# Kernel optimization log

Hardware: AMD Instinct MI355X
Metric: run time of the kernel (lower is better)

## Reference

```python
import jax, jax.numpy as jnp
import numpy as np


def setup_inputs() -> dict:
    key = jax.random.key(0)
    ks = jax.random.split(key, 5)
    B, H, W, C, R = 4, 64, 64, 256, 32
    x = jax.random.normal(ks[0], (B, H, W, C), dtype=jnp.float32)
    # 1x1 conv kernels stored as [C_in, C_out] matrices (equivalent math)
    w_f = jax.random.normal(ks[1], (C, R), dtype=jnp.float32) * (1.0 / np.sqrt(C))
    w_g = jax.random.normal(ks[2], (C, R), dtype=jnp.float32) * (1.0 / np.sqrt(C))
    w_h = jax.random.normal(ks[3], (C, R), dtype=jnp.float32) * (1.0 / np.sqrt(C))
    w_v = jax.random.normal(ks[4], (R, C), dtype=jnp.float32) * (1.0 / np.sqrt(R))
    gamma = jnp.zeros((1,), dtype=jnp.float32)
    return {"x": x, "w_f": w_f, "w_g": w_g, "w_h": w_h, "w_v": w_v, "gamma": gamma}


def reference(x, w_f, w_g, w_h, w_v, gamma):
    B, H, W, C = x.shape
    N = H * W
    xt = x.reshape(B, N, C)                       # flatten spatial tokens
    f = jnp.einsum('bnc,cr->bnr', xt, w_f)        # 1x1 conv == token-wise matmul
    g = jnp.einsum('bnc,cr->bnr', xt, w_g)
    h = jnp.einsum('bnc,cr->bnr', xt, w_h)
    scores = jnp.einsum('bnr,bmr->bnm', f, g)     # [B, N, N]
    # NOTE: original softmaxes over axis=1 (the query/row axis), not axis=-1
    attn = jax.nn.softmax(scores, axis=1)
    y = jnp.einsum('bnm,bmr->bnr', attn, h)       # [B, N, R]
    y = jnp.einsum('bnr,rc->bnc', y, w_v)         # output 1x1 conv
    y = y.reshape(B, H, W, C)
    return gamma * y + x
```

## Files before the change

kernel.cpp:

```cpp
#include <hip/hip_runtime.h>


#define BB 4
#define NN 4096
#define CC 256
#define RR 32
#define CSEG 4
#define MP 40
#define LOG2E 1.44269504088896340736f

typedef short short8 __attribute__((ext_vector_type(8)));
typedef unsigned short ushort8 __attribute__((ext_vector_type(8)));
typedef float floatx4 __attribute__((ext_vector_type(4)));

#define MFMA16 __builtin_amdgcn_mfma_f32_16x16x32_bf16

static __device__ __forceinline__ unsigned short f2bf(float f) {
  union { float f; unsigned u; } v; v.f = f;
  const unsigned r = v.u + 0x7fffu + ((v.u >> 16) & 1u);
  return (unsigned short)(r >> 16);
}
static __device__ __forceinline__ unsigned bfpack(float lo, float hi) {
  return __builtin_amdgcn_perm(__float_as_uint(hi), __float_as_uint(lo), 0x07060302u);
}

__global__ __launch_bounds__(256) void k_prep(
    const float* __restrict__ wf, const float* __restrict__ wg,
    const float* __restrict__ wh, const float* __restrict__ wv,
    unsigned short* __restrict__ wfrag, unsigned short* __restrict__ wvfrag) {
  const int idx = blockIdx.x * 256 + threadIdx.x;
  const int lane = (idx >> 3) & 63;
  const int j = idx & 7;
  const int col = lane & 15, q = lane >> 4;
  if (idx < 24576) {
    const int mat = idx >> 13;
    const int fid = (idx >> 9) & 15;
    const int kc = fid >> 1, nt = fid & 1;
    const float* w = (mat == 0) ? wf : ((mat == 1) ? wg : wh);
    wfrag[idx] = f2bf(w[(kc * 32 + q * 8 + j) * RR + nt * 16 + col]);
  } else {
    const int r = idx - 24576;
    const int t = (r >> 9) & 15;
    wvfrag[r] = f2bf(wv[(q * 8 + j) * CC + t * 16 + col]);
  }
}

__global__ __launch_bounds__(256) void k_fgh(
    const float* __restrict__ x, const unsigned short* __restrict__ wfrag,
    unsigned short* __restrict__ f16, unsigned short* __restrict__ g16,
    unsigned short* __restrict__ hT16) {
  __shared__ unsigned short wflds[24576];
  const int tid = threadIdx.x, lane = tid & 63, wave = tid >> 6;
  const int col = lane & 15, q = lane >> 4;
  {
    const uint4* src = (const uint4*)wfrag;
    uint4* dst = (uint4*)wflds;
#pragma unroll
    for (int i = 0; i < 12; ++i) dst[tid + i * 256] = src[tid + i * 256];
  }
  __syncthreads();
  const int t0 = blockIdx.x * 64 + wave * 16;
  short8 af[8];
  const float* xr = x + (long)(t0 + col) * CC + q * 8;
#pragma unroll
  for (int kc = 0; kc < 8; ++kc) {
    float tmp[8];
    *(float4*)(tmp) = *(const float4*)(xr + kc * 32);
    *(float4*)(tmp + 4) = *(const float4*)(xr + kc * 32 + 4);
    short8 o;
#pragma unroll
    for (int j = 0; j < 8; ++j) o[j] = (short)f2bf(tmp[j]);
    af[kc] = o;
  }
  const floatx4 zero = {0.f, 0.f, 0.f, 0.f};
  floatx4 acc[3][2];
#pragma unroll
  for (int m = 0; m < 3; ++m) { acc[m][0] = zero; acc[m][1] = zero; }
#pragma unroll
  for (int kc = 0; kc < 8; ++kc) {
#pragma unroll
    for (int mat = 0; mat < 3; ++mat) {
#pragma unroll
      for (int nt = 0; nt < 2; ++nt) {
        const short8 bf = *(const short8*)(wflds + (mat * 16 + kc * 2 + nt) * 512 + lane * 8);
        acc[mat][nt] = MFMA16(af[kc], bf, acc[mat][nt], 0, 0, 0);
      }
    }
  }
  const int b = t0 >> 12;
#pragma unroll
  for (int nt = 0; nt < 2; ++nt) {
#pragma unroll
    for (int r = 0; r < 4; ++r) {
      const int tok = t0 + q * 4 + r;
      const int n = nt * 16 + col;
      f16[(long)tok * RR + n] = f2bf(acc[0][nt][r] * LOG2E);
      g16[(long)tok * RR + n] = f2bf(acc[1][nt][r]);
      hT16[((long)b * RR + n) * NN + (tok & (NN - 1))] = f2bf(acc[2][nt][r]);
    }
  }
}

__global__ __launch_bounds__(256) void k_colsum(
    const unsigned short* __restrict__ f16, const unsigned short* __restrict__ g16,
    float* __restrict__ psum) {
  const int tid = threadIdx.x, lane = tid & 63, wave = tid >> 6;
  const int col = lane & 15, q = lane >> 4;
  const int mblk = blockIdx.x & 31;
  const int b = (blockIdx.x >> 5) & 3;
  const int seg = blockIdx.x >> 7;
  const int m0 = mblk * 128 + wave * 32;
  const short8 bg1 = *(const short8*)(g16 + ((long)(b * NN + m0 + col)) * RR + q * 8);
  const short8 bg2 = *(const short8*)(g16 + ((long)(b * NN + m0 + 16 + col)) * RR + q * 8);
  const floatx4 zero = {0.f, 0.f, 0.f, 0.f};
  float s1 = 0.f, s2 = 0.f;
  const unsigned short* fb = f16 + ((long)b * NN + seg * (NN / CSEG)) * RR;
#pragma unroll 4
  for (int n = 0; n < NN / CSEG; n += 16) {
    const short8 af = *(const short8*)(fb + (long)(n + col) * RR + q * 8);
    const floatx4 d1 = MFMA16(af, bg1, zero, 0, 0, 0);
    const floatx4 d2 = MFMA16(af, bg2, zero, 0, 0, 0);
    s1 += __builtin_amdgcn_exp2f(d1[0]) + __builtin_amdgcn_exp2f(d1[1]) +
          __builtin_amdgcn_exp2f(d1[2]) + __builtin_amdgcn_exp2f(d1[3]);
    s2 += __builtin_amdgcn_exp2f(d2[0]) + __builtin_amdgcn_exp2f(d2[1]) +
          __builtin_amdgcn_exp2f(d2[2]) + __builtin_amdgcn_exp2f(d2[3]);
  }
  s1 += __shfl_xor(s1, 16); s1 += __shfl_xor(s1, 32);
  s2 += __shfl_xor(s2, 16); s2 += __shfl_xor(s2, 32);
  if (lane < 16) {
    psum[(long)seg * (BB * NN) + b * NN + m0 + lane] = s1;
    psum[(long)seg * (BB * NN) + b * NN + m0 + 16 + lane] = s2;
  }
}

__global__ __launch_bounds__(256) void k_scaleh(
    const float* __restrict__ psum, unsigned short* __restrict__ hT16) {
  const long i8 = ((long)blockIdx.x * 256 + threadIdx.x) * 8;
  const int b = (int)(i8 >> 17);
  const int m = (int)(i8 & (NN - 1));
  float cs[8] = {0.f, 0.f, 0.f, 0.f, 0.f, 0.f, 0.f, 0.f};
#pragma unroll
  for (int sg = 0; sg < CSEG; ++sg) {
    const float* p = psum + (long)sg * (BB * NN) + b * NN + m;
    const float4 a = *(const float4*)p;
    const float4 c = *(const float4*)(p + 4);
    cs[0] += a.x; cs[1] += a.y; cs[2] += a.z; cs[3] += a.w;
    cs[4] += c.x; cs[5] += c.y; cs[6] += c.z; cs[7] += c.w;
  }
  const ushort8 hv = *(const ushort8*)(hT16 + i8);
  ushort8 o;
#pragma unroll
  for (int j = 0; j < 8; ++j) {
    const float h = __uint_as_float(((unsigned)hv[j]) << 16);
    o[j] = f2bf(h * __builtin_amdgcn_rcpf(cs[j]));
  }
  *(ushort8*)(hT16 + i8) = o;
}

#define C_ADDR(TN, TM) (((TN) + col) * MP + (TM) + q * 4)
__global__ __launch_bounds__(512, 4) void k_pvout(
    const unsigned short* __restrict__ f16, const unsigned short* __restrict__ g16,
    const unsigned short* __restrict__ hT16, const unsigned short* __restrict__ wvfrag,
    const float* __restrict__ x, const float* __restrict__ gamma,
    float* __restrict__ out) {
  __shared__ float ylds[8][32 * 36];
  __shared__ unsigned short pt_all[8][32 * MP];
  const int tid = threadIdx.x, lane = tid & 63, wave = tid >> 6;
  const int col = lane & 15, q = lane >> 4;
  const int b = blockIdx.x >> 7;
  const int t0 = (blockIdx.x & 127) * 32;
  const floatx4 zero = {0.f, 0.f, 0.f, 0.f};
  const short8 af1 = *(const short8*)(f16 + ((long)(b * NN + t0 + col)) * RR + q * 8);
  const short8 af2 = *(const short8*)(f16 + ((long)(b * NN + t0 + 16 + col)) * RR + q * 8);
  floatx4 a11 = zero, a12 = zero, a21 = zero, a22 = zero;
  unsigned short* pt = &pt_all[wave][0];
  const unsigned short* gb = g16 + (long)b * NN * RR;
  const unsigned short* hb = hT16 + (long)b * RR * NN;
  const int mq = wave * 512;
#pragma unroll 2
  for (int mi = 0; mi < 512; mi += 32) {
    const int m0 = mq + mi;
    const short8 bg1 = *(const short8*)(gb + (long)(m0 + col) * RR + q * 8);
    const short8 bg2 = *(const short8*)(gb + (long)(m0 + 16 + col) * RR + q * 8);
    const floatx4 d00 = MFMA16(bg1, af1, zero, 0, 0, 0);
    const floatx4 d01 = MFMA16(bg2, af1, zero, 0, 0, 0);
    const floatx4 d10 = MFMA16(bg1, af2, zero, 0, 0, 0);
    const floatx4 d11 = MFMA16(bg2, af2, zero, 0, 0, 0);
    float w0, w1, w2, w3;
    w0 = __builtin_amdgcn_exp2f(d00[0]); w1 = __builtin_amdgcn_exp2f(d00[1]);
    w2 = __builtin_amdgcn_exp2f(d00[2]); w3 = __builtin_amdgcn_exp2f(d00[3]);
    *(uint2*)(pt + C_ADDR(0, 0)) = make_uint2(bfpack(w0, w1), bfpack(w2, w3));
    w0 = __builtin_amdgcn_exp2f(d01[0]); w1 = __builtin_amdgcn_exp2f(d01[1]);
    w2 = __builtin_amdgcn_exp2f(d01[2]); w3 = __builtin_amdgcn_exp2f(d01[3]);
    *(uint2*)(pt + C_ADDR(0, 16)) = make_uint2(bfpack(w0, w1), bfpack(w2, w3));
    w0 = __builtin_amdgcn_exp2f(d10[0]); w1 = __builtin_amdgcn_exp2f(d10[1]);
    w2 = __builtin_amdgcn_exp2f(d10[2]); w3 = __builtin_amdgcn_exp2f(d10[3]);
    *(uint2*)(pt + C_ADDR(16, 0)) = make_uint2(bfpack(w0, w1), bfpack(w2, w3));
    w0 = __builtin_amdgcn_exp2f(d11[0]); w1 = __builtin_amdgcn_exp2f(d11[1]);
    w2 = __builtin_amdgcn_exp2f(d11[2]); w3 = __builtin_amdgcn_exp2f(d11[3]);
    *(uint2*)(pt + C_ADDR(16, 16)) = make_uint2(bfpack(w0, w1), bfpack(w2, w3));
    const short8 ap1 = *(const short8*)(pt + col * MP + q * 8);
    const short8 ap2 = *(const short8*)(pt + (col + 16) * MP + q * 8);
    const short8 bh1 = *(const short8*)(hb + (long)col * NN + m0 + q * 8);
    const short8 bh2 = *(const short8*)(hb + (long)(col + 16) * NN + m0 + q * 8);
    a11 = MFMA16(ap1, bh1, a11, 0, 0, 0);
    a12 = MFMA16(ap1, bh2, a12, 0, 0, 0);
    a21 = MFMA16(ap2, bh1, a21, 0, 0, 0);
    a22 = MFMA16(ap2, bh2, a22, 0, 0, 0);
  }
  {
    float* yp = &ylds[wave][0];
#pragma unroll
    for (int r = 0; r < 4; ++r) {
      yp[(q * 4 + r) * 36 + col] = a11[r];
      yp[(q * 4 + r) * 36 + col + 16] = a12[r];
      yp[(16 + q * 4 + r) * 36 + col] = a21[r];
      yp[(16 + q * 4 + r) * 36 + col + 16] = a22[r];
    }
  }
  __syncthreads();
  {
    const int tile = wave & 1, hh = wave >> 1;
    float s[8] = {0.f, 0.f, 0.f, 0.f, 0.f, 0.f, 0.f, 0.f};
#pragma unroll
    for (int w2 = 0; w2 < 8; ++w2) {
      const float* yp = &ylds[w2][(tile * 16 + col) * 36 + q * 8];
      const float4 u0 = *(const float4*)yp;
      const float4 u1 = *(const float4*)(yp + 4);
      s[0] += u0.x; s[1] += u0.y; s[2] += u0.z; s[3] += u0.w;
      s[4] += u1.x; s[5] += u1.y; s[6] += u1.z; s[7] += u1.w;
    }
    short8 ay;
#pragma unroll
    for (int j = 0; j < 8; ++j) ay[j] = (short)f2bf(s[j]);
    const float gm = gamma[0];
    float* sc = (float*)pt;
    const int row = lane >> 2, c4 = (lane & 3) * 4;
#pragma unroll
    for (int tp = 0; tp < 4; tp += 2) {
      const short8 bw0 = *(const short8*)(wvfrag + (hh * 4 + tp) * 512 + lane * 8);
      const short8 bw1 = *(const short8*)(wvfrag + (hh * 4 + tp + 1) * 512 + lane * 8);
      const floatx4 d0 = MFMA16(ay, bw0, zero, 0, 0, 0);
      const floatx4 d1 = MFMA16(ay, bw1, zero, 0, 0, 0);
#pragma unroll
      for (int r = 0; r < 4; ++r) {
        sc[(q * 4 + r) * 36 + col] = d0[r];
        sc[(q * 4 + r) * 36 + col + 16] = d1[r];
      }
#pragma unroll
      for (int j = 0; j < 2; ++j) {
        const float4 v = *(const float4*)(sc + row * 36 + c4 + j * 16);
        const long gidx = (long)(b * NN + t0 + tile * 16 + row) * CC +
                          hh * 64 + tp * 16 + j * 16 + c4;
        const float4 xv = *(const float4*)(x + gidx);
        float4 o;
        o.x = gm * v.x + xv.x; o.y = gm * v.y + xv.y;
        o.z = gm * v.z + xv.z; o.w = gm * v.w + xv.w;
        *(float4*)(out + gidx) = o;
      }
    }
  }
}

extern "C" void kernel_launch(void* const* d_in, const int* in_sizes, int n_in,
                              void* d_out, int out_size, void* d_ws, size_t ws_size,
                              hipStream_t stream) {
  const float* x = (const float*)d_in[0];
  const float* wf = (const float*)d_in[1];
  const float* wg = (const float*)d_in[2];
  const float* wh = (const float*)d_in[3];
  const float* wv = (const float*)d_in[4];
  const float* gamma = (const float*)d_in[5];
  float* out = (float*)d_out;

  unsigned short* f16 = (unsigned short*)d_ws;
  unsigned short* g16 = f16 + (long)BB * NN * RR;
  unsigned short* hT16 = g16 + (long)BB * NN * RR;
  unsigned short* wfrag = hT16 + (long)BB * NN * RR;
  unsigned short* wvfrag = wfrag + 24576;
  float* psum = (float*)(wvfrag + 8192);

  k_prep<<<128, 256, 0, stream>>>(wf, wg, wh, wv, wfrag, wvfrag);
  k_fgh<<<BB * NN / 64, 256, 0, stream>>>(x, wfrag, f16, g16, hT16);
  k_colsum<<<CSEG * BB * 32, 256, 0, stream>>>(f16, g16, psum);
  k_scaleh<<<BB * RR * NN / 2048, 256, 0, stream>>>(psum, hT16);
  k_pvout<<<BB * 128, 512, 0, stream>>>(f16, g16, hT16, wvfrag, x, gamma, out);
}
```

Before: 123.3 us.

## Feed exp scores directly from MFMA accumulators into PV MFMA, skipping LDS transpose

The P·V product now takes the exponentiated score accumulators straight from registers as A-operands of 16x16x16 bf16 MFMAs, so the per-iteration LDS store and reload of the P tile goes away. To match the register layout, the transposed h buffer is written in a permuted token order, and the column-sum normalisation kernel reads its sums with the same permutation. The cost is twice as many smaller-K MFMA instructions and a more intricate index mapping that must stay consistent across three kernels.

Result: no change. 125.0 us (+1.4%).

```diff
diff --git a/kernel.cpp b/kernel.cpp
--- a/kernel.cpp
+++ b/kernel.cpp
@@ -6,14 +6,15 @@
 #define CC 256
 #define RR 32
 #define CSEG 4
-#define MP 40
 #define LOG2E 1.44269504088896340736f
 
 typedef short short8 __attribute__((ext_vector_type(8)));
+typedef short short4v __attribute__((ext_vector_type(4)));
 typedef unsigned short ushort8 __attribute__((ext_vector_type(8)));
 typedef float floatx4 __attribute__((ext_vector_type(4)));
 
 #define MFMA16 __builtin_amdgcn_mfma_f32_16x16x32_bf16
+#define MFMA16K __builtin_amdgcn_mfma_f32_16x16x16bf16_1k
 
 static __device__ __forceinline__ unsigned short f2bf(float f) {
   union { float f; unsigned u; } v; v.f = f;
@@ -96,7 +97,9 @@
       const int n = nt * 16 + col;
       f16[(long)tok * RR + n] = f2bf(acc[0][nt][r] * LOG2E);
       g16[(long)tok * RR + n] = f2bf(acc[1][nt][r]);
-      hT16[((long)b * RR + n) * NN + (tok & (NN - 1))] = f2bf(acc[2][nt][r]);
+      const int tl = tok & (NN - 1);
+      const int sp = (tl & ~31) | (q << 3) | ((tl & 16) >> 2) | r;
+      hT16[((long)b * RR + n) * NN + sp] = f2bf(acc[2][nt][r]);
     }
   }
 }
@@ -138,12 +141,13 @@
   const long i8 = ((long)blockIdx.x * 256 + threadIdx.x) * 8;
   const int b = (int)(i8 >> 17);
   const int m = (int)(i8 & (NN - 1));
+  const int lo = (m & ~31) | ((m & 24) >> 1);
   float cs[8] = {0.f, 0.f, 0.f, 0.f, 0.f, 0.f, 0.f, 0.f};
 #pragma unroll
   for (int sg = 0; sg < CSEG; ++sg) {
-    const float* p = psum + (long)sg * (BB * NN) + b * NN + m;
-    const float4 a = *(const float4*)p;
-    const float4 c = *(const float4*)(p + 4);
+    const float* p = psum + (long)sg * (BB * NN) + b * NN;
+    const float4 a = *(const float4*)(p + lo);
+    const float4 c = *(const float4*)(p + lo + 16);
     cs[0] += a.x; cs[1] += a.y; cs[2] += a.z; cs[3] += a.w;
     cs[4] += c.x; cs[5] += c.y; cs[6] += c.z; cs[7] += c.w;
   }
@@ -157,14 +161,13 @@
   *(ushort8*)(hT16 + i8) = o;
 }
 
-#define C_ADDR(TN, TM) (((TN) + col) * MP + (TM) + q * 4)
 __global__ __launch_bounds__(512, 4) void k_pvout(
     const unsigned short* __restrict__ f16, const unsigned short* __restrict__ g16,
     const unsigned short* __restrict__ hT16, const unsigned short* __restrict__ wvfrag,
     const float* __restrict__ x, const float* __restrict__ gamma,
     float* __restrict__ out) {
   __shared__ float ylds[8][32 * 36];
-  __shared__ unsigned short pt_all[8][32 * MP];
+  __shared__ float sc_all[8][16 * 36];
   const int tid = threadIdx.x, lane = tid & 63, wave = tid >> 6;
   const int col = lane & 15, q = lane >> 4;
   const int b = blockIdx.x >> 7;
@@ -173,7 +176,6 @@
   const short8 af1 = *(const short8*)(f16 + ((long)(b * NN + t0 + col)) * RR + q * 8);
   const short8 af2 = *(const short8*)(f16 + ((long)(b * NN + t0 + 16 + col)) * RR + q * 8);
   floatx4 a11 = zero, a12 = zero, a21 = zero, a22 = zero;
-  unsigned short* pt = &pt_all[wave][0];
   const unsigned short* gb = g16 + (long)b * NN * RR;
   const unsigned short* hb = hT16 + (long)b * RR * NN;
   const int mq = wave * 512;
@@ -182,31 +184,33 @@
     const int m0 = mq + mi;
     const short8 bg1 = *(const short8*)(gb + (long)(m0 + col) * RR + q * 8);
     const short8 bg2 = *(const short8*)(gb + (long)(m0 + 16 + col) * RR + q * 8);
+    const short8 hv1 = *(const short8*)(hb + (long)col * NN + m0 + q * 8);
+    const short8 hv2 = *(const short8*)(hb + (long)(col + 16) * NN + m0 + q * 8);
     const floatx4 d00 = MFMA16(bg1, af1, zero, 0, 0, 0);
     const floatx4 d01 = MFMA16(bg2, af1, zero, 0, 0, 0);
     const floatx4 d10 = MFMA16(bg1, af2, zero, 0, 0, 0);
     const floatx4 d11 = MFMA16(bg2, af2, zero, 0, 0, 0);
-    float w0, w1, w2, w3;
-    w0 = __builtin_amdgcn_exp2f(d00[0]); w1 = __builtin_amdgcn_exp2f(d00[1]);
-    w2 = __builtin_amdgcn_exp2f(d00[2]); w3 = __builtin_amdgcn_exp2f(d00[3]);
-    *(uint2*)(pt + C_ADDR(0, 0)) = make_uint2(bfpack(w0, w1), bfpack(w2, w3));
-    w0 = __builtin_amdgcn_exp2f(d01[0]); w1 = __builtin_amdgcn_exp2f(d01[1]);
-    w2 = __builtin_amdgcn_exp2f(d01[2]); w3 = __builtin_amdgcn_exp2f(d01[3]);
-    *(uint2*)(pt + C_ADDR(0, 16)) = make_uint2(bfpack(w0, w1), bfpack(w2, w3));
-    w0 = __builtin_amdgcn_exp2f(d10[0]); w1 = __builtin_amdgcn_exp2f(d10[1]);
-    w2 = __builtin_amdgcn_exp2f(d10[2]); w3 = __builtin_amdgcn_exp2f(d10[3]);
-    *(uint2*)(pt + C_ADDR(16, 0)) = make_uint2(bfpack(w0, w1), bfpack(w2, w3));
-    w0 = __builtin_amdgcn_exp2f(d11[0]); w1 = __builtin_amdgcn_exp2f(d11[1]);
-    w2 = __builtin_amdgcn_exp2f(d11[2]); w3 = __builtin_amdgcn_exp2f(d11[3]);
-    *(uint2*)(pt + C_ADDR(16, 16)) = make_uint2(bfpack(w0, w1), bfpack(w2, w3));
-    const short8 ap1 = *(const short8*)(pt + col * MP + q * 8);
-    const short8 ap2 = *(const short8*)(pt + (col + 16) * MP + q * 8);
-    const short8 bh1 = *(const short8*)(hb + (long)col * NN + m0 + q * 8);
-    const short8 bh2 = *(const short8*)(hb + (long)(col + 16) * NN + m0 + q * 8);
-    a11 = MFMA16(ap1, bh1, a11, 0, 0, 0);
-    a12 = MFMA16(ap1, bh2, a12, 0, 0, 0);
-    a21 = MFMA16(ap2, bh1, a21, 0, 0, 0);
-    a22 = MFMA16(ap2, bh2, a22, 0, 0, 0);
+    union PU { unsigned u[2]; short4v s; } p00, p01, p10, p11;
+    p00.u[0] = bfpack(__builtin_amdgcn_exp2f(d00[0]), __builtin_amdgcn_exp2f(d00[1]));
+    p00.u[1] = bfpack(__builtin_amdgcn_exp2f(d00[2]), __builtin_amdgcn_exp2f(d00[3]));
+    p01.u[0] = bfpack(__builtin_amdgcn_exp2f(d01[0]), __builtin_amdgcn_exp2f(d01[1]));
+    p01.u[1] = bfpack(__builtin_amdgcn_exp2f(d01[2]), __builtin_amdgcn_exp2f(d01[3]));
+    p10.u[0] = bfpack(__builtin_amdgcn_exp2f(d10[0]), __builtin_amdgcn_exp2f(d10[1]));
+    p10.u[1] = bfpack(__builtin_amdgcn_exp2f(d10[2]), __builtin_amdgcn_exp2f(d10[3]));
+    p11.u[0] = bfpack(__builtin_amdgcn_exp2f(d11[0]), __builtin_amdgcn_exp2f(d11[1]));
+    p11.u[1] = bfpack(__builtin_amdgcn_exp2f(d11[2]), __builtin_amdgcn_exp2f(d11[3]));
+    const short4v bh1lo = __builtin_shufflevector(hv1, hv1, 0, 1, 2, 3);
+    const short4v bh1hi = __builtin_shufflevector(hv1, hv1, 4, 5, 6, 7);
+    const short4v bh2lo = __builtin_shufflevector(hv2, hv2, 0, 1, 2, 3);
+    const short4v bh2hi = __builtin_shufflevector(hv2, hv2, 4, 5, 6, 7);
+    a11 = MFMA16K(p00.s, bh1lo, a11, 0, 0, 0);
+    a11 = MFMA16K(p01.s, bh1hi, a11, 0, 0, 0);
+    a12 = MFMA16K(p00.s, bh2lo, a12, 0, 0, 0);
+    a12 = MFMA16K(p01.s, bh2hi, a12, 0, 0, 0);
+    a21 = MFMA16K(p10.s, bh1lo, a21, 0, 0, 0);
+    a21 = MFMA16K(p11.s, bh1hi, a21, 0, 0, 0);
+    a22 = MFMA16K(p10.s, bh2lo, a22, 0, 0, 0);
+    a22 = MFMA16K(p11.s, bh2hi, a22, 0, 0, 0);
   }
   {
     float* yp = &ylds[wave][0];
@@ -234,7 +238,7 @@
 #pragma unroll
     for (int j = 0; j < 8; ++j) ay[j] = (short)f2bf(s[j]);
     const float gm = gamma[0];
-    float* sc = (float*)pt;
+    float* sc = &sc_all[wave][0];
     const int row = lane >> 2, c4 = (lane & 3) * 4;
 #pragma unroll
     for (int tp = 0; tp < 4; tp += 2) {
```
